# Kernel optimization log

Measured on AMD Instinct MI355X. Metric: run time of the kernel, lower is better.

Reference implementation:

```python
import jax, jax.numpy as jnp
import numpy as np
from jax import lax

B, N, C, D = 8, 512, 37, 2048          # frames, rois/frame, classes (incl. bg), feat dim
SCORE_THR = 0.1
NMS_THR = 0.4
BBOX_STDS = np.array([0.1, 0.1, 0.2, 0.2], dtype=np.float32)


def setup_inputs() -> dict:
    key = jax.random.key(0)
    k1, k2, k3, k4, k5, k6 = jax.random.split(key, 6)
    # rois: [batch_idx, x1, y1, x2, y2] in a 600x1000 image
    x1 = jax.random.uniform(k1, (B, N)) * 900.0
    y1 = jax.random.uniform(k2, (B, N)) * 500.0
    w = jax.random.uniform(k3, (B, N)) * 120.0 + 8.0
    h = jax.random.uniform(k4, (B, N)) * 120.0 + 8.0
    bidx = jnp.broadcast_to(jnp.arange(B, dtype=jnp.float32)[:, None], (B, N))
    rois = jnp.stack([bidx, x1, y1, x1 + w, y1 + h], axis=-1)  # [B,N,5]
    bbox_pred = jax.random.normal(k5, (B, N, 4 * C)) * 0.5
    scores = jax.nn.softmax(jax.random.normal(k6, (B, N, C)) * 2.0, axis=-1)
    im_info = jnp.tile(jnp.array([[600.0, 1000.0, 1.0]], dtype=jnp.float32), (B, 1))
    roi_features = jax.random.normal(jax.random.fold_in(key, 7), (B, N, D))
    return {"rois": rois, "bbox_pred": bbox_pred, "scores": scores,
            "im_info": im_info, "roi_features": roi_features}


def _iou_matrix(b):
    # b: [N,4] -> [N,N] pairwise IoU (torchvision nms convention, no +1)
    area = (b[:, 2] - b[:, 0]) * (b[:, 3] - b[:, 1])
    lt = jnp.maximum(b[:, None, :2], b[None, :, :2])
    rb = jnp.minimum(b[:, None, 2:], b[None, :, 2:])
    wh = jnp.clip(rb - lt, 0.0)
    inter = wh[..., 0] * wh[..., 1]
    return inter / (area[:, None] + area[None, :] - inter + 1e-9)


def _nms_one(boxes, scores):
    # boxes [N,4], scores [N] -> keep mask [N] (greedy NMS on score-thresholded boxes)
    n = boxes.shape[0]
    valid = scores > SCORE_THR
    order = jnp.argsort(-jnp.where(valid, scores, -jnp.inf))
    b = boxes[order]
    v = valid[order]
    iou = _iou_matrix(b)
    idx = jnp.arange(n)

    def body(i, keep):
        suppressed = jnp.any((iou[:, i] > NMS_THR) & keep & (idx < i))
        return keep.at[i].set(v[i] & ~suppressed)

    keep_sorted = lax.fori_loop(0, n, body, jnp.zeros(n, bool))
    return jnp.zeros(n, bool).at[order].set(keep_sorted)


def reference(rois, bbox_pred, scores, im_info, roi_features):
    stds = jnp.asarray(BBOX_STDS)
    deltas = bbox_pred.reshape(B, N, C, 4) * stds
    # bbox_transform_inv
    w = (rois[..., 3] - rois[..., 1])[..., None]             # [B,N,1]
    h = (rois[..., 4] - rois[..., 2])[..., None]
    cx = rois[..., 1][..., None] + 0.5 * w
    cy = rois[..., 2][..., None] + 0.5 * h
    px = deltas[..., 0] * w + cx
    py = deltas[..., 1] * h + cy
    pw = jnp.exp(deltas[..., 2]) * w
    ph = jnp.exp(deltas[..., 3]) * h
    x1 = px - 0.5 * pw
    y1 = py - 0.5 * ph
    x2 = px + 0.5 * pw
    y2 = py + 0.5 * ph
    # clip_boxes to image
    xmax = (im_info[:, 1] - 1.0)[:, None, None]
    ymax = (im_info[:, 0] - 1.0)[:, None, None]
    boxes = jnp.stack([jnp.clip(x1, 0.0, xmax), jnp.clip(y1, 0.0, ymax),
                       jnp.clip(x2, 0.0, xmax), jnp.clip(y2, 0.0, ymax)], axis=-1)  # [B,N,C,4]
    # foreground classes 1..C-1, class-major layout: [B,C-1,N,*]
    boxes_fg = jnp.moveaxis(boxes[:, :, 1:, :], 2, 1)        # [B,C-1,N,4]
    scores_fg = jnp.moveaxis(scores[:, :, 1:], 2, 1)         # [B,C-1,N]
    keep = jax.vmap(jax.vmap(_nms_one))(boxes_fg, scores_fg)  # [B,C-1,N] bool
    cls_dets = jnp.where(keep[..., None],
                         jnp.concatenate([boxes_fg, scores_fg[..., None]], axis=-1),
                         0.0)                                 # [B,C-1,N,5]
    kept_feats = jnp.where(jnp.any(keep, axis=1)[..., None], roi_features, 0.0)  # [B,N,D]
    return cls_dets, kept_feats, keep
```

## Files before the change

kernel.cpp:

```cpp
#include <hip/hip_runtime.h>
#include <math.h>

#define BATCH 8
#define BN    512
#define NC    37
#define NFG   36
#define FD    2048


__global__ __launch_bounds__(64) void nms_kernel(
    const float* __restrict__ rois,
    const float* __restrict__ bbox_pred,
    const float* __restrict__ scores,
    const float* __restrict__ im_info,
    float* __restrict__ cls_dets,
    float* __restrict__ keep_out,
    int*   __restrict__ anykeep)
{
    const int bc   = blockIdx.x;
    const int b    = bc / NFG;
    const int cc   = bc % NFG;
    const int c    = cc + 1;
    const int lane = threadIdx.x;

    __shared__ float sb[BN][4];
    __shared__ float sarea[BN];
    __shared__ float cscore[BN];
    __shared__ int   cn[BN];
    __shared__ float kflag[BN];
    __shared__ unsigned char srem[BN];

    const float xmax = im_info[b * 3 + 1] - 1.0f;
    const float ymax = im_info[b * 3 + 0] - 1.0f;
    const unsigned long long lmask_lt = (lane == 0) ? 0ull : ((1ull << lane) - 1ull);

    float sc[8];
#pragma unroll
    for (int r = 0; r < 8; ++r) {
        const int n = r * 64 + lane;
        sc[r] = scores[(size_t)(b * BN + n) * NC + c];
        kflag[n] = 0.0f;
    }
    int base = 0;
#pragma unroll
    for (int r = 0; r < 8; ++r) {
        const int n = r * 64 + lane;
        const bool valid = sc[r] > 0.1f;
        const unsigned long long m = __ballot(valid);
        if (valid) {
            const int pos = base + __popcll(m & lmask_lt);
            cscore[pos] = sc[r];
            cn[pos] = n;
            const float* rr = rois + (size_t)(b * BN + n) * 5;
            const float x1r = rr[1], y1r = rr[2], x2r = rr[3], y2r = rr[4];
            const float w  = x2r - x1r;
            const float h  = y2r - y1r;
            const float cx = x1r + 0.5f * w;
            const float cy = y1r + 0.5f * h;
            const float* dp = bbox_pred + (size_t)(b * BN + n) * (4 * NC) + 4 * c;
            const float px = (dp[0] * 0.1f) * w + cx;
            const float py = (dp[1] * 0.1f) * h + cy;
            const float pw = expf(dp[2] * 0.2f) * w;
            const float ph = expf(dp[3] * 0.2f) * h;
            float bx1 = fminf(fmaxf(px - 0.5f * pw, 0.0f), xmax);
            float by1 = fminf(fmaxf(py - 0.5f * ph, 0.0f), ymax);
            float bx2 = fminf(fmaxf(px + 0.5f * pw, 0.0f), xmax);
            float by2 = fminf(fmaxf(py + 0.5f * ph, 0.0f), ymax);
            sb[n][0] = bx1; sb[n][1] = by1; sb[n][2] = bx2; sb[n][3] = by2;
            sarea[n] = (bx2 - bx1) * (by2 - by1);
        }
        base += __popcll(m);
    }
    const int V = base;
    __syncthreads();

    if (V <= 64) {
        float key; int id;
        if (lane < V) { key = cscore[lane]; id = cn[lane]; }
        else          { key = -INFINITY;    id = BN + lane; }
#pragma unroll
        for (int k = 2; k <= 64; k <<= 1) {
#pragma unroll
            for (int j = k >> 1; j > 0; j >>= 1) {
                const float ok = __shfl_xor(key, j);
                const int   oi = __shfl_xor(id, j);
                const bool is_lower   = (lane & j) == 0;
                const bool dir_desc   = (lane & k) == 0;
                const bool mine_first = (key > ok) || (key == ok && id < oi);
                bool take = mine_first ^ is_lower;
                if (!dir_desc) take = !take;
                if (take) { key = ok; id = oi; }
            }
        }
        float x1 = 0, y1 = 0, x2 = 0, y2 = 0, ar = 0;
        if (lane < V) { x1 = sb[id][0]; y1 = sb[id][1]; x2 = sb[id][2]; y2 = sb[id][3]; ar = sarea[id]; }
        unsigned long long rem = (V == 64) ? ~0ull : ((1ull << V) - 1ull);
        for (int i = 0; i < V; ++i) {
            if (!((rem >> i) & 1ull)) continue;
            const float ax1 = __shfl(x1, i);
            const float ay1 = __shfl(y1, i);
            const float ax2 = __shfl(x2, i);
            const float ay2 = __shfl(y2, i);
            const float aar = __shfl(ar, i);
            const float ix1 = fmaxf(ax1, x1);
            const float iy1 = fmaxf(ay1, y1);
            const float ix2 = fminf(ax2, x2);
            const float iy2 = fminf(ay2, y2);
            const float iw = fmaxf(ix2 - ix1, 0.0f);
            const float ih = fmaxf(iy2 - iy1, 0.0f);
            const float inter = iw * ih;
            const float iou = inter / (aar + ar - inter + 1e-9f);
            const unsigned long long sup = __ballot((iou > 0.4f) && (lane > i));
            rem &= ~sup;
        }
        if (lane < V && ((rem >> lane) & 1ull)) {
            kflag[id] = key;
            anykeep[b * BN + id] = 1;
        }
    } else {
        int P = 64; while (P < V) P <<= 1;
        for (int i = lane; i < P; i += 64) {
            if (i >= V) { cscore[i] = -INFINITY; cn[i] = BN + i; }
            srem[i] = (i < V) ? 1 : 0;
        }
        __syncthreads();
        for (int k = 2; k <= P; k <<= 1) {
            for (int j = k >> 1; j > 0; j >>= 1) {
                __syncthreads();
                for (int i = lane; i < P; i += 64) {
                    const int ixj = i ^ j;
                    if (ixj > i) {
                        const float ka = cscore[i], kb = cscore[ixj];
                        const int   ia = cn[i],     ib = cn[ixj];
                        const bool a_first = (ka > kb) || (ka == kb && ia < ib);
                        const bool up = ((i & k) == 0);
                        if (up ? !a_first : a_first) {
                            cscore[i] = kb; cscore[ixj] = ka;
                            cn[i] = ib;     cn[ixj] = ia;
                        }
                    }
                }
            }
        }
        __syncthreads();
        for (int i = 0; i < V; ++i) {
            __syncthreads();
            if (!srem[i]) continue;
            const int   ni  = cn[i];
            const float ax1 = sb[ni][0], ay1 = sb[ni][1];
            const float ax2 = sb[ni][2], ay2 = sb[ni][3];
            const float aar = sarea[ni];
            for (int jj = lane; jj < V; jj += 64) {
                if (jj > i && srem[jj]) {
                    const int nj = cn[jj];
                    const float ix1 = fmaxf(ax1, sb[nj][0]);
                    const float iy1 = fmaxf(ay1, sb[nj][1]);
                    const float ix2 = fminf(ax2, sb[nj][2]);
                    const float iy2 = fminf(ay2, sb[nj][3]);
                    const float iw = fmaxf(ix2 - ix1, 0.0f);
                    const float ih = fmaxf(iy2 - iy1, 0.0f);
                    const float inter = iw * ih;
                    const float iou = inter / (aar + sarea[nj] - inter + 1e-9f);
                    if (iou > 0.4f) srem[jj] = 0;
                }
            }
        }
        __syncthreads();
        for (int i = lane; i < V; i += 64) {
            if (srem[i]) {
                kflag[cn[i]] = cscore[i];
                anykeep[b * BN + cn[i]] = 1;
            }
        }
    }
    __syncthreads();

    const size_t rowbase = (size_t)(b * NFG + cc) * BN;
#pragma unroll
    for (int r = 0; r < 8; ++r) {
        const int n = r * 64 + lane;
        const float s = kflag[n];
        const bool kept = s > 0.0f;
        keep_out[rowbase + n] = kept ? 1.0f : 0.0f;
        float* cd = cls_dets + (rowbase + n) * 5;
        cd[0] = kept ? sb[n][0] : 0.0f;
        cd[1] = kept ? sb[n][1] : 0.0f;
        cd[2] = kept ? sb[n][2] : 0.0f;
        cd[3] = kept ? sb[n][3] : 0.0f;
        cd[4] = kept ? s : 0.0f;
    }
}

__global__ __launch_bounds__(256) void feat_kernel(
    const float* __restrict__ feats,
    const int*   __restrict__ anykeep,
    float* __restrict__ out_feats)
{
    const int bn = blockIdx.x;
    const int flag = anykeep[bn];
    const float4* src = (const float4*)(feats + (size_t)bn * FD);
    float4*       dst = (float4*)(out_feats + (size_t)bn * FD);
    if (flag) {
#pragma unroll
        for (int t = threadIdx.x; t < FD / 4; t += 256) dst[t] = src[t];
    } else {
        const float4 z = make_float4(0.f, 0.f, 0.f, 0.f);
#pragma unroll
        for (int t = threadIdx.x; t < FD / 4; t += 256) dst[t] = z;
    }
}

extern "C" void kernel_launch(void* const* d_in, const int* in_sizes, int n_in,
                              void* d_out, int out_size, void* d_ws, size_t ws_size,
                              hipStream_t stream) {
    const float* rois      = (const float*)d_in[0];
    const float* bbox_pred = (const float*)d_in[1];
    const float* scores    = (const float*)d_in[2];
    const float* im_info   = (const float*)d_in[3];
    const float* feats     = (const float*)d_in[4];

    float* out        = (float*)d_out;
    float* cls_dets   = out;
    float* kept_feats = out + (size_t)BATCH * NFG * BN * 5;
    float* keep_out   = kept_feats + (size_t)BATCH * BN * FD;

    int* anykeep = (int*)d_ws;
    hipMemsetAsync(anykeep, 0, (size_t)BATCH * BN * sizeof(int), stream);

    nms_kernel<<<BATCH * NFG, 64, 0, stream>>>(rois, bbox_pred, scores, im_info,
                                               cls_dets, keep_out, anykeep);
    feat_kernel<<<BATCH * BN, 256, 0, stream>>>(feats, anykeep, kept_feats);
}
```

Measured before the change: 112.1 us.

## Drop anykeep memset and batch box-decode loads ahead of compaction

Removes the workspace memset and the anykeep scatter writes. The feature kernel now derives the any-class keep flag by reading the 36 keep_out entries for its row into shared memory. Bbox deltas and ROI coordinates are loaded for all 8 rows up front, bbox deltas as a float4, and boxes are decoded for every ROI rather than only valid ones, so loads can overlap. This adds decode work for invalid boxes and 36 strided reads per feature block, in exchange for one fewer launch and coalesced, batched loads.

New measurement: 109.2 us. -2.6%, faster.

```diff
diff --git a/kernel.cpp b/kernel.cpp
--- a/kernel.cpp
+++ b/kernel.cpp
@@ -14,8 +14,7 @@
     const float* __restrict__ scores,
     const float* __restrict__ im_info,
     float* __restrict__ cls_dets,
-    float* __restrict__ keep_out,
-    int*   __restrict__ anykeep)
+    float* __restrict__ keep_out)
 {
     const int bc   = blockIdx.x;
     const int b    = bc / NFG;
@@ -34,13 +33,38 @@
     const float ymax = im_info[b * 3 + 0] - 1.0f;
     const unsigned long long lmask_lt = (lane == 0) ? 0ull : ((1ull << lane) - 1ull);
 
-    float sc[8];
+    float  sc[8];
+    float4 bp[8];
+    float  rx1[8], ry1[8], rx2[8], ry2[8];
 #pragma unroll
     for (int r = 0; r < 8; ++r) {
         const int n = r * 64 + lane;
         sc[r] = scores[(size_t)(b * BN + n) * NC + c];
+        bp[r] = *(const float4*)(bbox_pred + (size_t)(b * BN + n) * (4 * NC) + 4 * c);
+        const float* rr = rois + (size_t)(b * BN + n) * 5;
+        rx1[r] = rr[1]; ry1[r] = rr[2]; rx2[r] = rr[3]; ry2[r] = rr[4];
         kflag[n] = 0.0f;
     }
+
+#pragma unroll
+    for (int r = 0; r < 8; ++r) {
+        const int n = r * 64 + lane;
+        const float w  = rx2[r] - rx1[r];
+        const float h  = ry2[r] - ry1[r];
+        const float cx = rx1[r] + 0.5f * w;
+        const float cy = ry1[r] + 0.5f * h;
+        const float px = (bp[r].x * 0.1f) * w + cx;
+        const float py = (bp[r].y * 0.1f) * h + cy;
+        const float pw = expf(bp[r].z * 0.2f) * w;
+        const float ph = expf(bp[r].w * 0.2f) * h;
+        const float bx1 = fminf(fmaxf(px - 0.5f * pw, 0.0f), xmax);
+        const float by1 = fminf(fmaxf(py - 0.5f * ph, 0.0f), ymax);
+        const float bx2 = fminf(fmaxf(px + 0.5f * pw, 0.0f), xmax);
+        const float by2 = fminf(fmaxf(py + 0.5f * ph, 0.0f), ymax);
+        sb[n][0] = bx1; sb[n][1] = by1; sb[n][2] = bx2; sb[n][3] = by2;
+        sarea[n] = (bx2 - bx1) * (by2 - by1);
+    }
+
     int base = 0;
 #pragma unroll
     for (int r = 0; r < 8; ++r) {
@@ -51,23 +75,6 @@
             const int pos = base + __popcll(m & lmask_lt);
             cscore[pos] = sc[r];
             cn[pos] = n;
-            const float* rr = rois + (size_t)(b * BN + n) * 5;
-            const float x1r = rr[1], y1r = rr[2], x2r = rr[3], y2r = rr[4];
-            const float w  = x2r - x1r;
-            const float h  = y2r - y1r;
-            const float cx = x1r + 0.5f * w;
-            const float cy = y1r + 0.5f * h;
-            const float* dp = bbox_pred + (size_t)(b * BN + n) * (4 * NC) + 4 * c;
-            const float px = (dp[0] * 0.1f) * w + cx;
-            const float py = (dp[1] * 0.1f) * h + cy;
-            const float pw = expf(dp[2] * 0.2f) * w;
-            const float ph = expf(dp[3] * 0.2f) * h;
-            float bx1 = fminf(fmaxf(px - 0.5f * pw, 0.0f), xmax);
-            float by1 = fminf(fmaxf(py - 0.5f * ph, 0.0f), ymax);
-            float bx2 = fminf(fmaxf(px + 0.5f * pw, 0.0f), xmax);
-            float by2 = fminf(fmaxf(py + 0.5f * ph, 0.0f), ymax);
-            sb[n][0] = bx1; sb[n][1] = by1; sb[n][2] = bx2; sb[n][3] = by2;
-            sarea[n] = (bx2 - bx1) * (by2 - by1);
         }
         base += __popcll(m);
     }
@@ -115,7 +122,6 @@
         }
         if (lane < V && ((rem >> lane) & 1ull)) {
             kflag[id] = key;
-            anykeep[b * BN + id] = 1;
         }
     } else {
         int P = 64; while (P < V) P <<= 1;
@@ -167,10 +173,7 @@
         }
         __syncthreads();
         for (int i = lane; i < V; i += 64) {
-            if (srem[i]) {
-                kflag[cn[i]] = cscore[i];
-                anykeep[b * BN + cn[i]] = 1;
-            }
+            if (srem[i]) kflag[cn[i]] = cscore[i];
         }
     }
     __syncthreads();
@@ -193,14 +196,25 @@
 
 __global__ __launch_bounds__(256) void feat_kernel(
     const float* __restrict__ feats,
-    const int*   __restrict__ anykeep,
+    const float* __restrict__ keepf,
     float* __restrict__ out_feats)
 {
     const int bn = blockIdx.x;
-    const int flag = anykeep[bn];
+    const int b  = bn >> 9;
+    const int n  = bn & (BN - 1);
+
+    __shared__ int s_any;
+    if (threadIdx.x == 0) s_any = 0;
+    __syncthreads();
+    if (threadIdx.x < NFG) {
+        if (keepf[((size_t)b * NFG + threadIdx.x) * BN + n] != 0.0f)
+            s_any = 1;
+    }
+    __syncthreads();
+
     const float4* src = (const float4*)(feats + (size_t)bn * FD);
     float4*       dst = (float4*)(out_feats + (size_t)bn * FD);
-    if (flag) {
+    if (s_any) {
 #pragma unroll
         for (int t = threadIdx.x; t < FD / 4; t += 256) dst[t] = src[t];
     } else {
@@ -224,10 +238,7 @@
     float* kept_feats = out + (size_t)BATCH * NFG * BN * 5;
     float* keep_out   = kept_feats + (size_t)BATCH * BN * FD;
 
-    int* anykeep = (int*)d_ws;
-    hipMemsetAsync(anykeep, 0, (size_t)BATCH * BN * sizeof(int), stream);
-
     nms_kernel<<<BATCH * NFG, 64, 0, stream>>>(rois, bbox_pred, scores, im_info,
-                                               cls_dets, keep_out, anykeep);
-    feat_kernel<<<BATCH * BN, 256, 0, stream>>>(feats, anykeep, kept_feats);
+                                               cls_dets, keep_out);
+    feat_kernel<<<BATCH * BN, 256, 0, stream>>>(feats, keep_out, kept_feats);
 }
```
